# Kernel tuning notes

Measured on AMD Instinct MI355X. Metric: run time of the kernel, lower is better.

The kernel has to match this reference:

```python
import jax, jax.numpy as jnp
import numpy as np

B, S, D, H, V, N_SHARDS, CAP = 4, 512, 512, 8, 32000, 64, 128
HD = D // H


def _layernorm(x, g, b, eps=1e-5):
    mu = x.mean(-1, keepdims=True)
    var = ((x - mu) ** 2).mean(-1, keepdims=True)
    return (x - mu) * jax.lax.rsqrt(var + eps) * g + b


def setup_inputs() -> dict:
    key = jax.random.key(0)
    ks = jax.random.split(key, 16)
    s = 0.02
    return {
        'input_ids': jax.random.randint(ks[0], (B, S), 0, V, dtype=jnp.int32),
        'emb': jax.random.normal(ks[1], (V, D), jnp.float32) * s,
        'Wq': jax.random.normal(ks[2], (D, D), jnp.float32) * s,
        'Wk': jax.random.normal(ks[3], (D, D), jnp.float32) * s,
        'Wv': jax.random.normal(ks[4], (D, D), jnp.float32) * s,
        'Wo': jax.random.normal(ks[5], (D, D), jnp.float32) * s,
        'ln_g': jnp.ones((D,), jnp.float32),
        'ln_b': jnp.zeros((D,), jnp.float32),
        'W_router': jax.random.normal(ks[6], (D, N_SHARDS), jnp.float32),
        'mem_keys': jax.random.normal(ks[7], (N_SHARDS, CAP, D), jnp.float32) * s,
        'mem_values': jax.random.normal(ks[8], (N_SHARDS, CAP, D), jnp.float32) * s,
        'Wg_c': jax.random.normal(ks[9], (D, D), jnp.float32) * s,
        'Wg_m': jax.random.normal(ks[10], (D, D), jnp.float32) * s,
        'bg': jnp.zeros((D,), jnp.float32),
        'Wd': jax.random.normal(ks[11], (D, V), jnp.float32) * s,
        'bd': jnp.zeros((V,), jnp.float32),
        'top_k': 4,
    }


def reference(input_ids, emb, Wq, Wk, Wv, Wo, ln_g, ln_b, W_router,
              mem_keys, mem_values, Wg_c, Wg_m, bg, Wd, bd, top_k):
    # --- encode_context: embedding + causal MHA block (ContextSynthesizer) ---
    x = emb[input_ids]                                   # [B,S,D]
    q = (x @ Wq).reshape(B, S, H, HD)
    k = (x @ Wk).reshape(B, S, H, HD)
    v = (x @ Wv).reshape(B, S, H, HD)
    att = jnp.einsum('bqhd,bkhd->bhqk', q, k) / jnp.sqrt(jnp.float32(HD))
    causal = jnp.tril(jnp.ones((S, S), bool))
    att = jnp.where(causal[None, None], att, jnp.finfo(att.dtype).min)
    att = jax.nn.softmax(att, axis=-1)
    o = jnp.einsum('bhqk,bkhd->bqhd', att, v).reshape(B, S, D) @ Wo
    ctx = _layernorm(x + o, ln_g, ln_b)                  # [B,S,D]

    # --- LSHRouter: hyperplane projection -> shard id per token ---
    routes = jnp.argmax(ctx @ W_router, axis=-1)         # [B,S] int

    # --- MemoryShardStore.query, batched: per-token routed shard top-k read ---
    keys_g = mem_keys[routes]                            # [B,S,CAP,D] irregular gather
    scores = jnp.einsum('bscd,bsd->bsc', keys_g, ctx)    # [B,S,CAP]
    top_v, top_i = jax.lax.top_k(scores, top_k)          # [B,S,k]
    w = jax.nn.softmax(top_v, axis=-1)
    vals = mem_values[routes[:, :, None], top_i]         # [B,S,k,D]
    memory_stream = jnp.einsum('bsk,bskd->bsd', w, vals)

    # --- GatedMemoryFusion ---
    gate = jax.nn.sigmoid(ctx @ Wg_c + memory_stream @ Wg_m + bg)
    fused = gate * ctx + (1.0 - gate) * memory_stream

    # --- decoder; payload bias is zero (store holds no sequence_chunk records) ---
    logits = fused @ Wd + bd                             # [B,S,V]
    return logits
```

## Files before the change

kernel.cpp:

```cpp
#include <hip/hip_runtime.h>

typedef unsigned short u16;
typedef float f32x4 __attribute__((ext_vector_type(4)));
typedef short short8 __attribute__((ext_vector_type(8)));
typedef __bf16 bf16x8 __attribute__((ext_vector_type(8)));

#define B_  4
#define S_  512
#define D_  512
#define H_  8
#define HD_ 64
#define V_  32000
#define NSHARD_ 64
#define CAP_ 128
#define TOK_ (B_ * S_)

__device__ __forceinline__ float bf2f(u16 u) { return __uint_as_float(((unsigned)u) << 16); }
__device__ __forceinline__ u16 f2bf(float f) {
  unsigned u = __float_as_uint(f);
  u += 0x7FFFu + ((u >> 16) & 1u);
  return (u16)(u >> 16);
}

__device__ __forceinline__ f32x4 mfma16(short8 a, short8 b, f32x4 c) {
  return __builtin_amdgcn_mfma_f32_16x16x32_bf16(
      __builtin_bit_cast(bf16x8, a), __builtin_bit_cast(bf16x8, b), c, 0, 0, 0);
}

__device__ __forceinline__ void load_lds16(const void* g, void* l) {
  __builtin_amdgcn_global_load_lds(
      (const __attribute__((address_space(1))) void*)g,
      (__attribute__((address_space(3))) void*)l, 16, 0, 0);
}

template<int NS, bool ACC, int OM, bool CSKIP, bool CKLIM>
__global__ __launch_bounds__(256) void gemm_bt(
    const u16* __restrict__ Ah, const u16* __restrict__ Al, int ldA, long sA1, long sA2,
    const u16* __restrict__ Bh, const u16* __restrict__ Bl, int ldB, long sB1, long sB2,
    void* __restrict__ C0, void* __restrict__ C1, int ldC, long sC1, long sC2,
    int K, int z2n, float alpha)
{
  __shared__ u16 AsH[64 * 64];
  __shared__ u16 BsH[64 * 64];
  __shared__ u16 AsL[(NS == 3) ? 64 * 64 : 8];
  __shared__ u16 BsL[(NS == 3) ? 64 * 64 : 8];

  const int n0 = blockIdx.x * 64;
  const int m0 = blockIdx.y * 64;
  if (CSKIP && n0 > m0 + 63) return;

  const int z = blockIdx.z;
  const int z1 = z / z2n, z2 = z - z1 * z2n;
  const long baseA = (long)z1 * sA1 + (long)z2 * sA2;
  const long baseB = (long)z1 * sB1 + (long)z2 * sB2;
  const long baseC = (long)z1 * sC1 + (long)z2 * sC2;

  const int tid = threadIdx.x;
  const int lane = tid & 63;
  const int w = tid >> 6;
  const int wm = (w >> 1) * 32, wn = (w & 1) * 32;
  const int fr = lane & 15, kg = lane >> 4;

  const int srow = lane >> 3;
  const int schunk = (lane & 7) ^ srow;

  const u16* gAh = Ah + baseA + (long)(m0 + w * 16 + srow) * ldA + schunk * 8;
  const u16* gBh = Bh + baseB + (long)(n0 + w * 16 + srow) * ldB + schunk * 8;
  const u16* gAl = (NS == 3) ? (Al + baseA + (long)(m0 + w * 16 + srow) * ldA + schunk * 8) : nullptr;
  const u16* gBl = (NS == 3) ? (Bl + baseB + (long)(n0 + w * 16 + srow) * ldB + schunk * 8) : nullptr;
  u16* lAh = &AsH[(w * 16) * 64];
  u16* lBh = &BsH[(w * 16) * 64];
  u16* lAl = &AsL[(NS == 3) ? (w * 16) * 64 : 0];
  u16* lBl = &BsL[(NS == 3) ? (w * 16) * 64 : 0];

  const int kmax = CKLIM ? (m0 + 64) : K;

  f32x4 acc[2][2] = {};

  for (int k0 = 0; k0 < kmax; k0 += 64) {
    load_lds16(gAh + k0, lAh);
    load_lds16(gAh + k0 + 8 * ldA, lAh + 8 * 64);
    load_lds16(gBh + k0, lBh);
    load_lds16(gBh + k0 + 8 * ldB, lBh + 8 * 64);
    if (NS == 3) {
      load_lds16(gAl + k0, lAl);
      load_lds16(gAl + k0 + 8 * ldA, lAl + 8 * 64);
      load_lds16(gBl + k0, lBl);
      load_lds16(gBl + k0 + 8 * ldB, lBl + 8 * 64);
    }
    __syncthreads();

    short8 ah[2][2], bh[2][2], al[2][2], bl[2][2];
#pragma unroll
    for (int mi = 0; mi < 2; ++mi) {
      int row = wm + mi * 16 + fr;
#pragma unroll
      for (int ks = 0; ks < 2; ++ks) {
        int idx = row * 64 + ((ks * 32 + kg * 8) ^ ((fr & 7) << 3));
        ah[mi][ks] = *(const short8*)&AsH[idx];
        if (NS == 3) al[mi][ks] = *(const short8*)&AsL[idx];
      }
    }
#pragma unroll
    for (int ni = 0; ni < 2; ++ni) {
      int row = wn + ni * 16 + fr;
#pragma unroll
      for (int ks = 0; ks < 2; ++ks) {
        int idx = row * 64 + ((ks * 32 + kg * 8) ^ ((fr & 7) << 3));
        bh[ni][ks] = *(const short8*)&BsH[idx];
        if (NS == 3) bl[ni][ks] = *(const short8*)&BsL[idx];
      }
    }
#pragma unroll
    for (int ks = 0; ks < 2; ++ks)
#pragma unroll
      for (int mi = 0; mi < 2; ++mi)
#pragma unroll
        for (int ni = 0; ni < 2; ++ni) {
          acc[mi][ni] = mfma16(ah[mi][ks], bh[ni][ks], acc[mi][ni]);
          if (NS == 3) {
            acc[mi][ni] = mfma16(ah[mi][ks], bl[ni][ks], acc[mi][ni]);
            acc[mi][ni] = mfma16(al[mi][ks], bh[ni][ks], acc[mi][ni]);
          }
        }
    __syncthreads();
  }

#pragma unroll
  for (int mi = 0; mi < 2; ++mi)
#pragma unroll
    for (int ni = 0; ni < 2; ++ni) {
      int gnc = n0 + wn + ni * 16 + fr;
#pragma unroll
      for (int r = 0; r < 4; ++r) {
        int gm = m0 + wm + mi * 16 + kg * 4 + r;
        float v = acc[mi][ni][r] * alpha;
        long idx = baseC + (long)gm * ldC + gnc;
        if (OM == 0) {
          float* C = (float*)C0;
          C[idx] = ACC ? (C[idx] + v) : v;
        } else {
          u16 h = f2bf(v);
          ((u16*)C0)[idx] = h;
          ((u16*)C1)[idx] = f2bf(v - bf2f(h));
        }
      }
    }
}

__global__ __launch_bounds__(512, 2) void logits_gemm256_k(
    const u16* __restrict__ A, const u16* __restrict__ Bt,
    const float* __restrict__ bias, float* __restrict__ C)
{
  __shared__ u16 As[2][256 * 64];
  __shared__ u16 Bs[2][256 * 64];

  const int id = blockIdx.x;
  const int swz = (id & 7) * 125 + (id >> 3);
  const int n0 = (swz >> 3) * 256;
  const int m0 = (swz & 7) * 256;

  const int tid = threadIdx.x;
  const int lane = tid & 63;
  const int wid = tid >> 6;
  const int wr = wid >> 2, wc = wid & 3;
  const int fr = lane & 15, kg = lane >> 4;
  const int srow = lane >> 3;
  const int schunk = (lane & 7) ^ srow;

  f32x4 acc[8][4] = {};
  short8 pa0[4][2], pa1[4][2], pb0[2][2], pb1[2][2];

  auto stageA = [&](int kt, int h) {
#pragma unroll
    for (int j = 0; j < 2; ++j) {
      int r0 = j * 128 + h * 64 + wid * 8;
      load_lds16(A + (long)(m0 + r0 + srow) * D_ + kt * 64 + schunk * 8,
                 &As[kt & 1][r0 * 64]);
    }
  };
  auto stageB = [&](int kt, int h) {
#pragma unroll
    for (int j = 0; j < 2; ++j) {
      int r0 = (j * 2 + (wid >> 2)) * 64 + h * 32 + (wid & 3) * 8;
      load_lds16(Bt + (long)(n0 + r0 + srow) * D_ + kt * 64 + schunk * 8,
                 &Bs[kt & 1][r0 * 64]);
    }
  };
  auto readA = [&](short8 (&d)[4][2], int buf, int h) {
#pragma unroll
    for (int mi = 0; mi < 4; ++mi)
#pragma unroll
      for (int ks = 0; ks < 2; ++ks) {
        int row = wr * 128 + h * 64 + mi * 16 + fr;
        d[mi][ks] = *(const short8*)&As[buf][row * 64 +
                        ((ks * 32 + kg * 8) ^ ((fr & 7) << 3))];
      }
  };
  auto readB = [&](short8 (&d)[2][2], int buf, int h) {
#pragma unroll
    for (int ni = 0; ni < 2; ++ni)
#pragma unroll
      for (int ks = 0; ks < 2; ++ks) {
        int row = wc * 64 + h * 32 + ni * 16 + fr;
        d[ni][ks] = *(const short8*)&Bs[buf][row * 64 +
                        ((ks * 32 + kg * 8) ^ ((fr & 7) << 3))];
      }
  };
  auto quad = [&](short8 (&a)[4][2], short8 (&b)[2][2], int mb, int nb) {
#pragma unroll
    for (int ks = 0; ks < 2; ++ks)
#pragma unroll
      for (int mi = 0; mi < 4; ++mi)
#pragma unroll
        for (int ni = 0; ni < 2; ++ni)
          acc[mb + mi][nb + ni] = mfma16(a[mi][ks], b[ni][ks], acc[mb + mi][nb + ni]);
  };

#define SYNC_PRE()                                          \
  __builtin_amdgcn_sched_barrier(0);                        \
  __builtin_amdgcn_s_barrier();                             \
  asm volatile("s_waitcnt lgkmcnt(0)" ::: "memory");        \
  __builtin_amdgcn_sched_barrier(0);                        \
  __builtin_amdgcn_s_setprio(1);
#define SYNC_POST()                                         \
  __builtin_amdgcn_s_setprio(0);                            \
  __builtin_amdgcn_sched_barrier(0);                        \
  __builtin_amdgcn_s_barrier();                             \
  __builtin_amdgcn_sched_barrier(0);

  stageA(0, 0); stageB(0, 0); stageB(0, 1); stageA(0, 1);
  stageA(1, 0); stageB(1, 0); stageB(1, 1);
  __builtin_amdgcn_sched_barrier(0);
  asm volatile("s_waitcnt vmcnt(6)" ::: "memory");
  __builtin_amdgcn_s_barrier();
  __builtin_amdgcn_sched_barrier(0);

  for (int i = 0; i < 4; ++i) {
    const int t1 = 2 * i + 1, t2 = 2 * i + 2, t3 = 2 * i + 3;
    const bool st2 = (t2 < 8), st3 = (t3 < 8);

    readA(pa0, 0, 0); readB(pb0, 0, 0);
    stageA(t1, 1);
    SYNC_PRE(); quad(pa0, pb0, 0, 0); SYNC_POST();

    readB(pb1, 0, 1);
    if (st2) stageA(t2, 0);
    SYNC_PRE(); quad(pa0, pb1, 0, 2); SYNC_POST();

    readA(pa1, 0, 1);
    if (st2) stageB(t2, 0);
    SYNC_PRE(); quad(pa1, pb1, 4, 2); SYNC_POST();

    if (st2) stageB(t2, 1);
    __builtin_amdgcn_sched_barrier(0);
    if (st2) { asm volatile("s_waitcnt vmcnt(6)" ::: "memory"); }
    else     { asm volatile("s_waitcnt vmcnt(0)" ::: "memory"); }
    __builtin_amdgcn_s_barrier();
    __builtin_amdgcn_sched_barrier(0);
    __builtin_amdgcn_s_setprio(1);
    quad(pa1, pb0, 4, 0);
    SYNC_POST();

    readA(pa0, 1, 0); readB(pb0, 1, 0);
    if (st2) stageA(t2, 1);
    SYNC_PRE(); quad(pa0, pb0, 0, 0); SYNC_POST();

    readB(pb1, 1, 1);
    if (st3) stageA(t3, 0);
    SYNC_PRE(); quad(pa0, pb1, 0, 2); SYNC_POST();

    readA(pa1, 1, 1);
    if (st3) stageB(t3, 0);
    SYNC_PRE(); quad(pa1, pb1, 4, 2); SYNC_POST();

    if (st3) stageB(t3, 1);
    __builtin_amdgcn_sched_barrier(0);
    if (st3) { asm volatile("s_waitcnt vmcnt(6)" ::: "memory"); }
    else     { asm volatile("s_waitcnt vmcnt(0)" ::: "memory"); }
    __builtin_amdgcn_s_barrier();
    __builtin_amdgcn_sched_barrier(0);
    __builtin_amdgcn_s_setprio(1);
    quad(pa1, pb0, 4, 0);
    SYNC_POST();
  }
#undef SYNC_PRE
#undef SYNC_POST

#pragma unroll
  for (int ni = 0; ni < 4; ++ni) {
    int gnc = n0 + wc * 64 + ni * 16 + fr;
    float bv = bias[gnc];
#pragma unroll
    for (int mi = 0; mi < 8; ++mi)
#pragma unroll
      for (int r = 0; r < 4; ++r) {
        int gm = m0 + wr * 128 + mi * 16 + kg * 4 + r;
        C[(long)gm * V_ + gnc] = acc[mi][ni][r] + bv;
      }
  }
}

template<bool LO>
__global__ __launch_bounds__(256) void transpose_split_k(
    const float* __restrict__ W, int ldw,
    u16* __restrict__ oh, u16* __restrict__ ol)
{
  __shared__ float t[64][65];
  const int n0 = blockIdx.x * 64;
  const int k0 = blockIdx.y * 64;
  const int tid = threadIdx.x;
  {
    const int kk = tid >> 4;
    const int c4 = (tid & 15) * 4;
#pragma unroll
    for (int i = 0; i < 4; ++i) {
      f32x4 v = *(const f32x4*)(W + (long)(k0 + kk + i * 16) * ldw + n0 + c4);
      t[kk + i * 16][c4] = v[0];
      t[kk + i * 16][c4 + 1] = v[1];
      t[kk + i * 16][c4 + 2] = v[2];
      t[kk + i * 16][c4 + 3] = v[3];
    }
  }
  __syncthreads();
  {
    const int chunk = tid & 7;
    const int nn = tid >> 3;
#pragma unroll
    for (int j = 0; j < 2; ++j) {
      int n = nn + j * 32;
      u16 hbuf[8], lbuf[8];
#pragma unroll
      for (int e = 0; e < 8; ++e) {
        float fv = t[chunk * 8 + e][n];
        u16 h = f2bf(fv);
        hbuf[e] = h;
        if (LO) lbuf[e] = f2bf(fv - bf2f(h));
      }
      long ob = (long)(n0 + n) * 512 + k0 + chunk * 8;
      *(short8*)(oh + ob) = *(short8*)hbuf;
      if (LO) *(short8*)(ol + ob) = *(short8*)lbuf;
    }
  }
}

__global__ __launch_bounds__(256) void v_transpose_k(
    const u16* __restrict__ qh, const u16* __restrict__ ql,
    u16* __restrict__ vTh, u16* __restrict__ vTl)
{
  __shared__ u16 th[64][68];
  __shared__ u16 tl[64][68];
  const int z = blockIdx.y;
  const int b = z >> 3, h = z & 7;
  const int s0 = blockIdx.x * 64;
  const long ibase = ((long)(b * 512 + s0)) * 1536 + 1024 + h * 64;
  const int tid = threadIdx.x;
  {
    const int sr = tid >> 2;
    const int c8 = (tid & 3) * 16;
    const long src = ibase + (long)sr * 1536 + c8;
    *(short8*)&th[sr][c8]     = *(const short8*)(qh + src);
    *(short8*)&th[sr][c8 + 8] = *(const short8*)(qh + src + 8);
    *(short8*)&tl[sr][c8]     = *(const short8*)(ql + src);
    *(short8*)&tl[sr][c8 + 8] = *(const short8*)(ql + src + 8);
  }
  __syncthreads();
  {
    const int dr = tid >> 2;
    const int s8 = (tid & 3) * 16;
    u16 oh[16], ol[16];
#pragma unroll
    for (int j = 0; j < 16; ++j) { oh[j] = th[s8 + j][dr]; ol[j] = tl[s8 + j][dr]; }
    long ob = (long)z * 64 * 512 + (long)dr * 512 + s0 + s8;
    *(short8*)(vTh + ob)     = *(short8*)&oh[0];
    *(short8*)(vTh + ob + 8) = *(short8*)&oh[8];
    *(short8*)(vTl + ob)     = *(short8*)&ol[0];
    *(short8*)(vTl + ob + 8) = *(short8*)&ol[8];
  }
}

__global__ __launch_bounds__(128) void embed_k(const int* __restrict__ ids,
                                               const float* __restrict__ emb,
                                               float* __restrict__ x,
                                               u16* __restrict__ xh,
                                               u16* __restrict__ xl) {
  const int t = blockIdx.x;
  const long id = ids[t];
  const int c = threadIdx.x * 4;
  f32x4 v = *(const f32x4*)(emb + id * (long)D_ + c);
  *(f32x4*)(x + (long)t * D_ + c) = v;
  u16 hh[4], ll[4];
#pragma unroll
  for (int j = 0; j < 4; ++j) {
    u16 h = f2bf(v[j]);
    hh[j] = h;
    ll[j] = f2bf(v[j] - bf2f(h));
  }
  *(unsigned long long*)(xh + (long)t * D_ + c) = *(unsigned long long*)hh;
  *(unsigned long long*)(xl + (long)t * D_ + c) = *(unsigned long long*)ll;
}

__global__ __launch_bounds__(64) void softmax_causal_k(
    const float* __restrict__ att, u16* __restrict__ ph, u16* __restrict__ pl) {
  const int row = blockIdx.x;
  const int i = row & 511;
  const float* p = att + ((long)row << 9);
  const int lane = threadIdx.x;
  float vals[8];
  float m = -3.4e38f;
#pragma unroll
  for (int it = 0; it < 8; ++it) {
    vals[it] = -3.4e38f;
    if (it * 64 <= i) {
      int j = it * 64 + lane;
      float v = (j <= i) ? p[j] : -3.4e38f;
      vals[it] = v;
      m = fmaxf(m, v);
    }
  }
#pragma unroll
  for (int off = 32; off; off >>= 1) m = fmaxf(m, __shfl_xor(m, off));
  float s = 0.f;
#pragma unroll
  for (int it = 0; it < 8; ++it) {
    if (it * 64 <= i) {
      int j = it * 64 + lane;
      float e = (j <= i) ? expf(vals[it] - m) : 0.f;
      vals[it] = e;
      s += e;
    }
  }
#pragma unroll
  for (int off = 32; off; off >>= 1) s += __shfl_xor(s, off);
  float inv = 1.f / s;
#pragma unroll
  for (int it = 0; it < 8; ++it) {
    if (it * 64 <= i) {
      long ob = ((long)row << 9) + it * 64 + lane;
      float e = vals[it] * inv;
      u16 h = f2bf(e);
      ph[ob] = h;
      pl[ob] = f2bf(e - bf2f(h));
    }
  }
}

__global__ __launch_bounds__(256) void resid_ln_k(
    const float* __restrict__ x, const float* __restrict__ proj,
    const float* __restrict__ g, const float* __restrict__ b,
    float* __restrict__ ctxf, u16* __restrict__ ctxh)
{
  const int t = blockIdx.x;
  const int tid = threadIdx.x;
  __shared__ float red[8];
  const float* xr = x + (long)t * D_;
  const float* pr = proj + (long)t * D_;
  float v0 = xr[tid] + pr[tid];
  float v1 = xr[tid + 256] + pr[tid + 256];
  float s = v0 + v1, q = v0 * v0 + v1 * v1;
#pragma unroll
  for (int off = 32; off; off >>= 1) { s += __shfl_xor(s, off); q += __shfl_xor(q, off); }
  const int wave = tid >> 6, lane = tid & 63;
  if (lane == 0) { red[wave] = s; red[4 + wave] = q; }
  __syncthreads();
  s = red[0] + red[1] + red[2] + red[3];
  q = red[4] + red[5] + red[6] + red[7];
  float mu = s * (1.f / 512.f);
  float var = q * (1.f / 512.f) - mu * mu;
  float rs = rsqrtf(var + 1e-5f);
  float o0 = (v0 - mu) * rs * g[tid] + b[tid];
  float o1 = (v1 - mu) * rs * g[tid + 256] + b[tid + 256];
  long base = (long)t * D_;
  ctxf[base + tid] = o0;
  ctxf[base + tid + 256] = o1;
  ctxh[base + tid] = f2bf(o0);
  ctxh[base + tid + 256] = f2bf(o1);
}

__global__ __launch_bounds__(128) void route_mem_k(
    const float* __restrict__ ctxf, const float* __restrict__ Wr,
    const float* __restrict__ keys, const float* __restrict__ valsm,
    float* __restrict__ msf, u16* __restrict__ msh)
{
  const int t = blockIdx.x;
  const int tid = threadIdx.x;
  __shared__ float sctx[D_];
  __shared__ float spart[CAP_];
  __shared__ float sred2[2][64];
  __shared__ int s_route;
  __shared__ int sidx[4];
  __shared__ float sw[4];

  f32x4 cv = ((const f32x4*)(ctxf + (long)t * D_))[tid];
  ((f32x4*)sctx)[tid] = cv;
  __syncthreads();

  {
    const int c = tid & 63, half = tid >> 6;
    float accr = 0.f;
    const float* cp = sctx + half * 256;
    const float* wp = Wr + (long)(half * 256) * NSHARD_ + c;
    for (int d = 0; d < 256; ++d) accr += cp[d] * wp[(long)d * NSHARD_];
    sred2[half][c] = accr;
  }
  __syncthreads();
  if (tid < 64) {
    float v = sred2[0][tid] + sred2[1][tid];
    int idx = tid;
#pragma unroll
    for (int off = 32; off; off >>= 1) {
      float ov = __shfl_xor(v, off);
      int oi = __shfl_xor(idx, off);
      if (ov > v || (ov == v && oi < idx)) { v = ov; idx = oi; }
    }
    if (tid == 0) s_route = idx;
  }
  __syncthreads();
  const int route = s_route;

  {
    const float* krow = keys + ((long)route * CAP_ + tid) * D_;
    float sc = 0.f;
    for (int d0 = 0; d0 < D_; d0 += 4) {
      f32x4 kv = *(const f32x4*)(krow + d0);
      sc += sctx[d0] * kv[0] + sctx[d0 + 1] * kv[1] +
            sctx[d0 + 2] * kv[2] + sctx[d0 + 3] * kv[3];
    }
    spart[tid] = sc;
  }
  __syncthreads();

  for (int rep = 0; rep < 4; ++rep) {
    if (tid < 64) {
      float v1 = spart[tid]; int i1 = tid;
      float v2 = spart[tid + 64]; int i2 = tid + 64;
      float v; int idx;
      if (v2 > v1) { v = v2; idx = i2; } else { v = v1; idx = i1; }
#pragma unroll
      for (int off = 32; off; off >>= 1) {
        float ov = __shfl_xor(v, off);
        int oi = __shfl_xor(idx, off);
        if (ov > v || (ov == v && oi < idx)) { v = ov; idx = oi; }
      }
      if (tid == 0) { sidx[rep] = idx; sw[rep] = v; spart[idx] = -3.4e38f; }
    }
    __syncthreads();
  }

  float w0 = sw[0], w1 = sw[1], w2 = sw[2], w3 = sw[3];
  float mx = fmaxf(fmaxf(w0, w1), fmaxf(w2, w3));
  float e0 = expf(w0 - mx), e1 = expf(w1 - mx), e2 = expf(w2 - mx), e3 = expf(w3 - mx);
  float inv = 1.f / (e0 + e1 + e2 + e3);
  float wk[4] = {e0 * inv, e1 * inv, e2 * inv, e3 * inv};

  float a0 = 0, a1 = 0, a2 = 0, a3 = 0;
#pragma unroll
  for (int k = 0; k < 4; ++k) {
    const float* vr = valsm + ((long)route * CAP_ + sidx[k]) * D_ + tid * 4;
    f32x4 vv = *(const f32x4*)vr;
    float w = wk[k];
    a0 += w * vv[0]; a1 += w * vv[1]; a2 += w * vv[2]; a3 += w * vv[3];
  }
  long ob = (long)t * D_ + tid * 4;
  f32x4 of; of[0] = a0; of[1] = a1; of[2] = a2; of[3] = a3;
  *(f32x4*)(msf + ob) = of;
  u16 oh[4];
  oh[0] = f2bf(a0); oh[1] = f2bf(a1); oh[2] = f2bf(a2); oh[3] = f2bf(a3);
  *(unsigned long long*)(msh + ob) = *(unsigned long long*)oh;
}

__global__ __launch_bounds__(256) void gate_fuse_k(
    const float* __restrict__ g1, const float* __restrict__ bg,
    const float* __restrict__ ctxf, const float* __restrict__ msf,
    u16* __restrict__ fused)
{
  long base = ((long)blockIdx.x * 256 + threadIdx.x) * 4;
  f32x4 gv = *(const f32x4*)(g1 + base);
  f32x4 cv = *(const f32x4*)(ctxf + base);
  f32x4 mv = *(const f32x4*)(msf + base);
  int col = (int)(base & 511);
  u16 o[4];
#pragma unroll
  for (int j = 0; j < 4; ++j) {
    float g = 1.f / (1.f + expf(-(gv[j] + bg[col + j])));
    o[j] = f2bf(g * cv[j] + (1.f - g) * mv[j]);
  }
  *(unsigned long long*)(fused + base) = *(unsigned long long*)o;
}

extern "C" void kernel_launch(void* const* d_in, const int* in_sizes, int n_in,
                              void* d_out, int out_size, void* d_ws, size_t ws_size,
                              hipStream_t stream) {
  const int*   ids  = (const int*)d_in[0];
  const float* emb  = (const float*)d_in[1];
  const float* Wq   = (const float*)d_in[2];
  const float* Wk   = (const float*)d_in[3];
  const float* Wv   = (const float*)d_in[4];
  const float* Wo   = (const float*)d_in[5];
  const float* ln_g = (const float*)d_in[6];
  const float* ln_b = (const float*)d_in[7];
  const float* Wr   = (const float*)d_in[8];
  const float* mk   = (const float*)d_in[9];
  const float* mv   = (const float*)d_in[10];
  const float* Wgc  = (const float*)d_in[11];
  const float* Wgm  = (const float*)d_in[12];
  const float* bg   = (const float*)d_in[13];
  const float* Wd   = (const float*)d_in[14];
  const float* bd   = (const float*)d_in[15];
  float* out = (float*)d_out;

  char* ws = (char*)d_ws;
  size_t off = 0;
  auto alloc = [&](size_t bytes) -> void* {
    void* p = ws + off;
    off += (bytes + 255) & ~(size_t)255;
    return p;
  };
  float* x      = (float*)alloc((size_t)TOK_ * D_ * 4);
  u16*   xh     = (u16*)  alloc((size_t)TOK_ * D_ * 2);
  u16*   xl     = (u16*)  alloc((size_t)TOK_ * D_ * 2);
  u16*   wqkvTh = (u16*)  alloc((size_t)3 * D_ * D_ * 2);
  u16*   wqkvTl = (u16*)  alloc((size_t)3 * D_ * D_ * 2);
  u16*   woTh   = (u16*)  alloc((size_t)D_ * D_ * 2);
  u16*   woTl   = (u16*)  alloc((size_t)D_ * D_ * 2);
  u16*   wgcTh  = (u16*)  alloc((size_t)D_ * D_ * 2);
  u16*   wgmTh  = (u16*)  alloc((size_t)D_ * D_ * 2);
  u16*   wdT    = (u16*)  alloc((size_t)D_ * V_ * 2);
  u16*   qkvh   = (u16*)  alloc((size_t)TOK_ * 3 * D_ * 2);
  u16*   qkvl   = (u16*)  alloc((size_t)TOK_ * 3 * D_ * 2);
  u16*   vTh    = (u16*)  alloc((size_t)B_ * H_ * HD_ * S_ * 2);
  u16*   vTl    = (u16*)  alloc((size_t)B_ * H_ * HD_ * S_ * 2);
  float* att    = (float*)alloc((size_t)B_ * H_ * S_ * S_ * 4);
  u16*   ph     = (u16*)  alloc((size_t)B_ * H_ * S_ * S_ * 2);
  u16*   pl     = (u16*)  alloc((size_t)B_ * H_ * S_ * S_ * 2);
  u16*   oh     = (u16*)  alloc((size_t)TOK_ * D_ * 2);
  u16*   ol     = (u16*)  alloc((size_t)TOK_ * D_ * 2);
  float* proj   = (float*)alloc((size_t)TOK_ * D_ * 4);
  float* ctxf   = (float*)alloc((size_t)TOK_ * D_ * 4);
  u16*   ctxh   = (u16*)  alloc((size_t)TOK_ * D_ * 2);
  float* msf    = (float*)alloc((size_t)TOK_ * D_ * 4);
  u16*   msh    = (u16*)  alloc((size_t)TOK_ * D_ * 2);
  float* g1     = (float*)alloc((size_t)TOK_ * D_ * 4);
  u16*   fused  = (u16*)  alloc((size_t)TOK_ * D_ * 2);

  {
    dim3 g8(D_ / 64, D_ / 64, 1);
    transpose_split_k<true><<<g8, 256, 0, stream>>>(Wq, D_, wqkvTh, wqkvTl);
    transpose_split_k<true><<<g8, 256, 0, stream>>>(Wk, D_, wqkvTh + D_ * D_, wqkvTl + D_ * D_);
    transpose_split_k<true><<<g8, 256, 0, stream>>>(Wv, D_, wqkvTh + 2 * D_ * D_, wqkvTl + 2 * D_ * D_);
    transpose_split_k<true><<<g8, 256, 0, stream>>>(Wo, D_, woTh, woTl);
    transpose_split_k<false><<<g8, 256, 0, stream>>>(Wgc, D_, wgcTh, nullptr);
    transpose_split_k<false><<<g8, 256, 0, stream>>>(Wgm, D_, wgmTh, nullptr);
    dim3 gd(V_ / 64, D_ / 64, 1);
    transpose_split_k<false><<<gd, 256, 0, stream>>>(Wd, V_, wdT, nullptr);
  }

  embed_k<<<TOK_, 128, 0, stream>>>(ids, emb, x, xh, xl);

  {
    dim3 g(1536 / 64, TOK_ / 64, 1);
    gemm_bt<3, false, 1, false, false><<<g, 256, 0, stream>>>(
        xh, xl, D_, 0, 0, wqkvTh, wqkvTl, D_, 0, 0,
        qkvh, qkvl, 1536, 0, 0, D_, 1, 1.f);
  }

  {
    dim3 g(S_ / 64, B_ * H_, 1);
    v_transpose_k<<<g, 256, 0, stream>>>(qkvh, qkvl, vTh, vTl);
  }

  {
    dim3 g(S_ / 64, S_ / 64, B_ * H_);
    gemm_bt<3, false, 0, true, false><<<g, 256, 0, stream>>>(
        qkvh, qkvl, 1536, (long)S_ * 1536, 64,
        qkvh + D_, qkvl + D_, 1536, (long)S_ * 1536, 64,
        att, nullptr, S_, (long)H_ * S_ * S_, (long)S_ * S_,
        HD_, H_, 0.125f);
  }

  softmax_causal_k<<<B_ * H_ * S_, 64, 0, stream>>>(att, ph, pl);

  {
    dim3 g(1, S_ / 64, B_ * H_);
    gemm_bt<3, false, 1, false, true><<<g, 256, 0, stream>>>(
        ph, pl, S_, (long)H_ * S_ * S_, (long)S_ * S_,
        vTh, vTl, S_, (long)H_ * HD_ * S_, (long)HD_ * S_,
        oh, ol, D_, (long)S_ * D_, HD_,
        S_, H_, 1.f);
  }

  {
    dim3 g(D_ / 64, TOK_ / 64, 1);
    gemm_bt<3, false, 0, false, false><<<g, 256, 0, stream>>>(
        oh, ol, D_, 0, 0, woTh, woTl, D_, 0, 0,
        proj, nullptr, D_, 0, 0, D_, 1, 1.f);
  }

  resid_ln_k<<<TOK_, 256, 0, stream>>>(x, proj, ln_g, ln_b, ctxf, ctxh);

  route_mem_k<<<TOK_, 128, 0, stream>>>(ctxf, Wr, mk, mv, msf, msh);

  {
    dim3 g(D_ / 64, TOK_ / 64, 1);
    gemm_bt<1, false, 0, false, false><<<g, 256, 0, stream>>>(
        ctxh, nullptr, D_, 0, 0, wgcTh, nullptr, D_, 0, 0,
        g1, nullptr, D_, 0, 0, D_, 1, 1.f);
    gemm_bt<1, true, 0, false, false><<<g, 256, 0, stream>>>(
        msh, nullptr, D_, 0, 0, wgmTh, nullptr, D_, 0, 0,
        g1, nullptr, D_, 0, 0, D_, 1, 1.f);
  }

  gate_fuse_k<<<(TOK_ * D_) / (256 * 4), 256, 0, stream>>>(g1, bg, ctxf, msf, fused);

  logits_gemm256_k<<<1000, 512, 0, stream>>>(fused, wdT, bd, out);
}
```

Before: 348.5 us.

## Specialize QK^T kernel, vectorize softmax, and merge the two gate GEMMs

Replaces the generic tiled GEMM for the attention scores with a dedicated kernel that loads its K=64 Q/K fragments straight from global memory into registers, with no LDS staging. It also rewrites the causal softmax so each lane handles 8 contiguous columns with vector loads and stores. The two gate GEMMs (ctx@Wg_c and mem@Wg_m) are merged into a single K=1024 GEMM over a concatenated activation buffer and concatenated transposed weights, which removes the accumulate pass over g1. The risks are uncoalesced direct global loads in the QK^T kernel and softmax writes that are now zero-padded to 64-column granularity.

```diff
diff --git a/kernel.cpp b/kernel.cpp
--- a/kernel.cpp
+++ b/kernel.cpp
@@ -33,7 +33,7 @@
       (__attribute__((address_space(3))) void*)l, 16, 0, 0);
 }
 
-template<int NS, bool ACC, int OM, bool CSKIP, bool CKLIM>
+template<int NS, bool ACC, int OM, bool CKLIM>
 __global__ __launch_bounds__(256) void gemm_bt(
     const u16* __restrict__ Ah, const u16* __restrict__ Al, int ldA, long sA1, long sA2,
     const u16* __restrict__ Bh, const u16* __restrict__ Bl, int ldB, long sB1, long sB2,
@@ -47,7 +47,6 @@
 
   const int n0 = blockIdx.x * 64;
   const int m0 = blockIdx.y * 64;
-  if (CSKIP && n0 > m0 + 63) return;
 
   const int z = blockIdx.z;
   const int z1 = z / z2n, z2 = z - z1 * z2n;
@@ -148,6 +147,68 @@
     }
 }
 
+__global__ __launch_bounds__(256) void qkt_k(
+    const u16* __restrict__ qkvh, const u16* __restrict__ qkvl,
+    float* __restrict__ att)
+{
+  const int n0 = blockIdx.x * 64;
+  const int m0 = blockIdx.y * 64;
+  if (n0 > m0 + 63) return;
+  const int z = blockIdx.z;
+  const int b = z >> 3, h = z & 7;
+  const long qbase = (long)b * 512 * 1536 + h * 64;
+  const long kbase = qbase + 512;
+  const long cbase = (long)z * 512 * 512;
+
+  const int tid = threadIdx.x;
+  const int lane = tid & 63;
+  const int w = tid >> 6;
+  const int wm = (w >> 1) * 32, wn = (w & 1) * 32;
+  const int fr = lane & 15, kg = lane >> 4;
+
+  short8 ah[2][2], al[2][2], bh[2][2], bl[2][2];
+#pragma unroll
+  for (int mi = 0; mi < 2; ++mi)
+#pragma unroll
+    for (int ks = 0; ks < 2; ++ks) {
+      long ra = qbase + (long)(m0 + wm + mi * 16 + fr) * 1536 + ks * 32 + kg * 8;
+      ah[mi][ks] = *(const short8*)(qkvh + ra);
+      al[mi][ks] = *(const short8*)(qkvl + ra);
+    }
+#pragma unroll
+  for (int ni = 0; ni < 2; ++ni)
+#pragma unroll
+    for (int ks = 0; ks < 2; ++ks) {
+      long rb = kbase + (long)(n0 + wn + ni * 16 + fr) * 1536 + ks * 32 + kg * 8;
+      bh[ni][ks] = *(const short8*)(qkvh + rb);
+      bl[ni][ks] = *(const short8*)(qkvl + rb);
+    }
+
+  f32x4 acc[2][2] = {};
+#pragma unroll
+  for (int ks = 0; ks < 2; ++ks)
+#pragma unroll
+    for (int mi = 0; mi < 2; ++mi)
+#pragma unroll
+      for (int ni = 0; ni < 2; ++ni) {
+        acc[mi][ni] = mfma16(ah[mi][ks], bh[ni][ks], acc[mi][ni]);
+        acc[mi][ni] = mfma16(ah[mi][ks], bl[ni][ks], acc[mi][ni]);
+        acc[mi][ni] = mfma16(al[mi][ks], bh[ni][ks], acc[mi][ni]);
+      }
+
+#pragma unroll
+  for (int mi = 0; mi < 2; ++mi)
+#pragma unroll
+    for (int ni = 0; ni < 2; ++ni) {
+      int gnc = n0 + wn + ni * 16 + fr;
+#pragma unroll
+      for (int r = 0; r < 4; ++r) {
+        int gm = m0 + wm + mi * 16 + kg * 4 + r;
+        att[cbase + (long)gm * 512 + gnc] = acc[mi][ni][r] * 0.125f;
+      }
+    }
+}
+
 __global__ __launch_bounds__(512, 2) void logits_gemm256_k(
     const u16* __restrict__ A, const u16* __restrict__ Bt,
     const float* __restrict__ bias, float* __restrict__ C)
@@ -303,7 +364,7 @@
 
 template<bool LO>
 __global__ __launch_bounds__(256) void transpose_split_k(
-    const float* __restrict__ W, int ldw,
+    const float* __restrict__ W, int ldw, int ldo, int koff,
     u16* __restrict__ oh, u16* __restrict__ ol)
 {
   __shared__ float t[64][65];
@@ -337,7 +398,7 @@
         hbuf[e] = h;
         if (LO) lbuf[e] = f2bf(fv - bf2f(h));
       }
-      long ob = (long)(n0 + n) * 512 + k0 + chunk * 8;
+      long ob = (long)(n0 + n) * ldo + koff + k0 + chunk * 8;
       *(short8*)(oh + ob) = *(short8*)hbuf;
       if (LO) *(short8*)(ol + ob) = *(short8*)lbuf;
     }
@@ -404,51 +465,58 @@
     const float* __restrict__ att, u16* __restrict__ ph, u16* __restrict__ pl) {
   const int row = blockIdx.x;
   const int i = row & 511;
-  const float* p = att + ((long)row << 9);
+  const long base = (long)row << 9;
+  const float* p = att + base;
   const int lane = threadIdx.x;
-  float vals[8];
+  const int c0 = lane * 8;
+  float v[8];
   float m = -3.4e38f;
-#pragma unroll
-  for (int it = 0; it < 8; ++it) {
-    vals[it] = -3.4e38f;
-    if (it * 64 <= i) {
-      int j = it * 64 + lane;
-      float v = (j <= i) ? p[j] : -3.4e38f;
-      vals[it] = v;
-      m = fmaxf(m, v);
-    }
+  if (c0 <= i) {
+    f32x4 a = *(const f32x4*)(p + c0);
+    f32x4 b2 = *(const f32x4*)(p + c0 + 4);
+#pragma unroll
+    for (int j = 0; j < 8; ++j) {
+      float x = (j < 4) ? a[j] : b2[j - 4];
+      x = (c0 + j <= i) ? x : -3.4e38f;
+      v[j] = x;
+      m = fmaxf(m, x);
+    }
+  } else {
+#pragma unroll
+    for (int j = 0; j < 8; ++j) v[j] = 0.f;
   }
 #pragma unroll
   for (int off = 32; off; off >>= 1) m = fmaxf(m, __shfl_xor(m, off));
   float s = 0.f;
-#pragma unroll
-  for (int it = 0; it < 8; ++it) {
-    if (it * 64 <= i) {
-      int j = it * 64 + lane;
-      float e = (j <= i) ? expf(vals[it] - m) : 0.f;
-      vals[it] = e;
+  if (c0 <= i) {
+#pragma unroll
+    for (int j = 0; j < 8; ++j) {
+      float e = (c0 + j <= i) ? expf(v[j] - m) : 0.f;
+      v[j] = e;
       s += e;
     }
   }
 #pragma unroll
   for (int off = 32; off; off >>= 1) s += __shfl_xor(s, off);
   float inv = 1.f / s;
-#pragma unroll
-  for (int it = 0; it < 8; ++it) {
-    if (it * 64 <= i) {
-      long ob = ((long)row << 9) + it * 64 + lane;
-      float e = vals[it] * inv;
+  if (c0 <= (i | 63)) {
+    u16 hh[8], ll[8];
+#pragma unroll
+    for (int j = 0; j < 8; ++j) {
+      float e = (c0 <= i) ? v[j] * inv : 0.f;
       u16 h = f2bf(e);
-      ph[ob] = h;
-      pl[ob] = f2bf(e - bf2f(h));
-    }
+      hh[j] = h;
+      ll[j] = f2bf(e - bf2f(h));
+    }
+    *(short8*)(ph + base + c0) = *(short8*)hh;
+    *(short8*)(pl + base + c0) = *(short8*)ll;
   }
 }
 
 __global__ __launch_bounds__(256) void resid_ln_k(
     const float* __restrict__ x, const float* __restrict__ proj,
     const float* __restrict__ g, const float* __restrict__ b,
-    float* __restrict__ ctxf, u16* __restrict__ ctxh)
+    float* __restrict__ ctxf, u16* __restrict__ catA)
 {
   const int t = blockIdx.x;
   const int tid = threadIdx.x;
@@ -473,14 +541,15 @@
   long base = (long)t * D_;
   ctxf[base + tid] = o0;
   ctxf[base + tid + 256] = o1;
-  ctxh[base + tid] = f2bf(o0);
-  ctxh[base + tid + 256] = f2bf(o1);
+  long cb = (long)t * 1024;
+  catA[cb + tid] = f2bf(o0);
+  catA[cb + tid + 256] = f2bf(o1);
 }
 
 __global__ __launch_bounds__(128) void route_mem_k(
     const float* __restrict__ ctxf, const float* __restrict__ Wr,
     const float* __restrict__ keys, const float* __restrict__ valsm,
-    float* __restrict__ msf, u16* __restrict__ msh)
+    float* __restrict__ msf, u16* __restrict__ catA)
 {
   const int t = blockIdx.x;
   const int tid = threadIdx.x;
@@ -561,12 +630,12 @@
     float w = wk[k];
     a0 += w * vv[0]; a1 += w * vv[1]; a2 += w * vv[2]; a3 += w * vv[3];
   }
-  long ob = (long)t * D_ + tid * 4;
   f32x4 of; of[0] = a0; of[1] = a1; of[2] = a2; of[3] = a3;
-  *(f32x4*)(msf + ob) = of;
+  *(f32x4*)(msf + (long)t * D_ + tid * 4) = of;
   u16 oh[4];
   oh[0] = f2bf(a0); oh[1] = f2bf(a1); oh[2] = f2bf(a2); oh[3] = f2bf(a3);
-  *(unsigned long long*)(msh + ob) = *(unsigned long long*)oh;
+  *(unsigned long long*)(catA + (long)t * 1024 + 512 + tid * 4) =
+      *(unsigned long long*)oh;
 }
 
 __global__ __launch_bounds__(256) void gate_fuse_k(
@@ -623,8 +692,7 @@
   u16*   wqkvTl = (u16*)  alloc((size_t)3 * D_ * D_ * 2);
   u16*   woTh   = (u16*)  alloc((size_t)D_ * D_ * 2);
   u16*   woTl   = (u16*)  alloc((size_t)D_ * D_ * 2);
-  u16*   wgcTh  = (u16*)  alloc((size_t)D_ * D_ * 2);
-  u16*   wgmTh  = (u16*)  alloc((size_t)D_ * D_ * 2);
+  u16*   wgT    = (u16*)  alloc((size_t)D_ * 1024 * 2);
   u16*   wdT    = (u16*)  alloc((size_t)D_ * V_ * 2);
   u16*   qkvh   = (u16*)  alloc((size_t)TOK_ * 3 * D_ * 2);
   u16*   qkvl   = (u16*)  alloc((size_t)TOK_ * 3 * D_ * 2);
@@ -637,29 +705,28 @@
   u16*   ol     = (u16*)  alloc((size_t)TOK_ * D_ * 2);
   float* proj   = (float*)alloc((size_t)TOK_ * D_ * 4);
   float* ctxf   = (float*)alloc((size_t)TOK_ * D_ * 4);
-  u16*   ctxh   = (u16*)  alloc((size_t)TOK_ * D_ * 2);
+  u16*   catA   = (u16*)  alloc((size_t)TOK_ * 1024 * 2);
   float* msf    = (float*)alloc((size_t)TOK_ * D_ * 4);
-  u16*   msh    = (u16*)  alloc((size_t)TOK_ * D_ * 2);
   float* g1     = (float*)alloc((size_t)TOK_ * D_ * 4);
   u16*   fused  = (u16*)  alloc((size_t)TOK_ * D_ * 2);
 
   {
     dim3 g8(D_ / 64, D_ / 64, 1);
-    transpose_split_k<true><<<g8, 256, 0, stream>>>(Wq, D_, wqkvTh, wqkvTl);
-    transpose_split_k<true><<<g8, 256, 0, stream>>>(Wk, D_, wqkvTh + D_ * D_, wqkvTl + D_ * D_);
-    transpose_split_k<true><<<g8, 256, 0, stream>>>(Wv, D_, wqkvTh + 2 * D_ * D_, wqkvTl + 2 * D_ * D_);
-    transpose_split_k<true><<<g8, 256, 0, stream>>>(Wo, D_, woTh, woTl);
-    transpose_split_k<false><<<g8, 256, 0, stream>>>(Wgc, D_, wgcTh, nullptr);
-    transpose_split_k<false><<<g8, 256, 0, stream>>>(Wgm, D_, wgmTh, nullptr);
+    transpose_split_k<true><<<g8, 256, 0, stream>>>(Wq, D_, 512, 0, wqkvTh, wqkvTl);
+    transpose_split_k<true><<<g8, 256, 0, stream>>>(Wk, D_, 512, 0, wqkvTh + D_ * D_, wqkvTl + D_ * D_);
+    transpose_split_k<true><<<g8, 256, 0, stream>>>(Wv, D_, 512, 0, wqkvTh + 2 * D_ * D_, wqkvTl + 2 * D_ * D_);
+    transpose_split_k<true><<<g8, 256, 0, stream>>>(Wo, D_, 512, 0, woTh, woTl);
+    transpose_split_k<false><<<g8, 256, 0, stream>>>(Wgc, D_, 1024, 0, wgT, nullptr);
+    transpose_split_k<false><<<g8, 256, 0, stream>>>(Wgm, D_, 1024, 512, wgT, nullptr);
     dim3 gd(V_ / 64, D_ / 64, 1);
-    transpose_split_k<false><<<gd, 256, 0, stream>>>(Wd, V_, wdT, nullptr);
+    transpose_split_k<false><<<gd, 256, 0, stream>>>(Wd, V_, 512, 0, wdT, nullptr);
   }
 
   embed_k<<<TOK_, 128, 0, stream>>>(ids, emb, x, xh, xl);
 
   {
     dim3 g(1536 / 64, TOK_ / 64, 1);
-    gemm_bt<3, false, 1, false, false><<<g, 256, 0, stream>>>(
+    gemm_bt<3, false, 1, false><<<g, 256, 0, stream>>>(
         xh, xl, D_, 0, 0, wqkvTh, wqkvTl, D_, 0, 0,
         qkvh, qkvl, 1536, 0, 0, D_, 1, 1.f);
   }
@@ -671,18 +738,14 @@
 
   {
     dim3 g(S_ / 64, S_ / 64, B_ * H_);
-    gemm_bt<3, false, 0, true, false><<<g, 256, 0, stream>>>(
-        qkvh, qkvl, 1536, (long)S_ * 1536, 64,
-        qkvh + D_, qkvl + D_, 1536, (long)S_ * 1536, 64,
-        att, nullptr, S_, (long)H_ * S_ * S_, (long)S_ * S_,
-        HD_, H_, 0.125f);
+    qkt_k<<<g, 256, 0, stream>>>(qkvh, qkvl, att);
   }
 
   softmax_causal_k<<<B_ * H_ * S_, 64, 0, stream>>>(att, ph, pl);
 
   {
     dim3 g(1, S_ / 64, B_ * H_);
-    gemm_bt<3, false, 1, false, true><<<g, 256, 0, stream>>>(
+    gemm_bt<3, false, 1, true><<<g, 256, 0, stream>>>(
         ph, pl, S_, (long)H_ * S_ * S_, (long)S_ * S_,
         vTh, vTl, S_, (long)H_ * HD_ * S_, (long)HD_ * S_,
         oh, ol, D_, (long)S_ * D_, HD_,
@@ -691,23 +754,20 @@
 
   {
     dim3 g(D_ / 64, TOK_ / 64, 1);
-    gemm_bt<3, false, 0, false, false><<<g, 256, 0, stream>>>(
+    gemm_bt<3, false, 0, false><<<g, 256, 0, stream>>>(
         oh, ol, D_, 0, 0, woTh, woTl, D_, 0, 0,
         proj, nullptr, D_, 0, 0, D_, 1, 1.f);
   }
 
-  resid_ln_k<<<TOK_, 256, 0, stream>>>(x, proj, ln_g, ln_b, ctxf, ctxh);
-
-  route_mem_k<<<TOK_, 128, 0, stream>>>(ctxf, Wr, mk, mv, msf, msh);
+  resid_ln_k<<<TOK_, 256, 0, stream>>>(x, proj, ln_g, ln_b, ctxf, catA);
+
+  route_mem_k<<<TOK_, 128, 0, stream>>>(ctxf, Wr, mk, mv, msf, catA);
 
   {
     dim3 g(D_ / 64, TOK_ / 64, 1);
-    gemm_bt<1, false, 0, false, false><<<g, 256, 0, stream>>>(
-        ctxh, nullptr, D_, 0, 0, wgcTh, nullptr, D_, 0, 0,
-        g1, nullptr, D_, 0, 0, D_, 1, 1.f);
-    gemm_bt<1, true, 0, false, false><<<g, 256, 0, stream>>>(
-        msh, nullptr, D_, 0, 0, wgmTh, nullptr, D_, 0, 0,
-        g1, nullptr, D_, 0, 0, D_, 1, 1.f);
+    gemm_bt<1, false, 0, false><<<g, 256, 0, stream>>>(
+        catA, nullptr, 1024, 0, 0, wgT, nullptr, 1024, 0, 0,
+        g1, nullptr, D_, 0, 0, 1024, 1, 1.f);
   }
 
   gate_fuse_k<<<(TOK_ * D_) / (256 * 4), 256, 0, stream>>>(g1, bg, ctxf, msf, fused);
```

New measurement: 350.2 us. About the same (+0.5%).
